# Kernel tuning notes

Hardware: AMD Instinct MI355X
Metric: run time of the kernel (lower is better)

## Reference

```python
import jax, jax.numpy as jnp
import numpy as np

N = 8192
IN_DIM = 256
OUT_DIM = 256  # out_dim//num_heads * num_heads == out_dim
EDGE_PROB = 0.01


def setup_inputs() -> dict:
    key = jax.random.key(0)
    k_adj, k_h, k_q, k_k, k_v = jax.random.split(key, 5)
    # Dense 0/1 adjacency mask, multiplied into the score matrix.
    adj = (jax.random.uniform(k_adj, (N, N)) < EDGE_PROB).astype(jnp.float32)
    h = jax.random.normal(k_h, (N, IN_DIM), dtype=jnp.float32)
    # torch nn.Linear stores weight as [out_features, in_features]; no bias (use_bias=False).
    s = 1.0 / np.sqrt(IN_DIM)
    Wq = jax.random.normal(k_q, (OUT_DIM, IN_DIM), dtype=jnp.float32) * s
    Wk = jax.random.normal(k_k, (OUT_DIM, IN_DIM), dtype=jnp.float32) * s
    Wv = jax.random.normal(k_v, (OUT_DIM, IN_DIM), dtype=jnp.float32) * s
    return {"adj": adj, "h": h, "Wq": Wq, "Wk": Wk, "Wv": Wv}


def reference(adj, h, Wq, Wk, Wv):
    # Q_h, K_h, V_h: [N, out_dim]
    Q_h = h @ Wq.T
    K_h = h @ Wk.T
    V_h = h @ Wv.T
    scale = 1.0 / jnp.sqrt(jnp.asarray(h.shape[1], dtype=h.dtype))
    # Scores masked multiplicatively by adjacency (faithful to source: zeros,
    # not -inf, so non-edges still contribute exp(0) after softmax).
    A_tilde = scale * (Q_h @ K_h.T) * adj            # [N, N]
    attention = jax.nn.softmax(A_tilde, axis=1)       # softmax over dim 1
    X_tilde = attention @ V_h                         # [N, out_dim]
    return X_tilde
```

## Files before the change

kernel.cpp:

```cpp
#include <hip/hip_runtime.h>


#define NN  8192
#define DIM 256
#define SCALE 0.0625f
#define CAP 128

typedef __attribute__((ext_vector_type(8))) short short8;
typedef __attribute__((ext_vector_type(4))) float f32x4;
typedef __attribute__((ext_vector_type(4))) unsigned int u32x4;

__device__ __forceinline__ unsigned short f2bf(float f) {
    union { float f; unsigned u; } v; v.f = f;
    unsigned u = v.u;
    unsigned r = (u + 0x7fffu + ((u >> 16) & 1u)) >> 16;
    return (unsigned short)r;
}
__device__ __forceinline__ float bf2f(unsigned short s) {
    union { unsigned u; float f; } v; v.u = ((unsigned)s) << 16;
    return v.f;
}
__device__ __forceinline__ float dw_lo(unsigned u) {
    union { unsigned u; float f; } v; v.u = u << 16; return v.f;
}
__device__ __forceinline__ float dw_hi(unsigned u) {
    union { unsigned u; float f; } v; v.u = u & 0xffff0000u; return v.f;
}

__global__ __launch_bounds__(256) void prep_kernel(
    const float* __restrict__ h, const float* __restrict__ Wq,
    const float* __restrict__ Wk, const float* __restrict__ Wv,
    unsigned short* __restrict__ h_bf, unsigned short* __restrict__ w_bf)
{
    int b = blockIdx.x, t = threadIdx.x;
    if (b < 2048) {
        int idx = (b * 256 + t) * 4;
        float4 v = *(const float4*)(h + idx);
        ushort4 o; o.x = f2bf(v.x); o.y = f2bf(v.y); o.z = f2bf(v.z); o.w = f2bf(v.w);
        *(ushort4*)(h_bf + idx) = o;
    } else {
        int idx = ((b - 2048) * 256 + t) * 4;
        int w = idx >> 16;
        int offn = idx & 65535;
        const float* src = (w == 0) ? Wq : (w == 1) ? Wk : Wv;
        float4 v = *(const float4*)(src + offn);
        ushort4 o; o.x = f2bf(v.x); o.y = f2bf(v.y); o.z = f2bf(v.z); o.w = f2bf(v.w);
        *(ushort4*)(w_bf + idx) = o;
    }
}

__global__ __launch_bounds__(256) void proj_gemm(
    const unsigned short* __restrict__ h_bf, const unsigned short* __restrict__ w_bf,
    float* __restrict__ Q, unsigned short* __restrict__ Kb, unsigned short* __restrict__ Vb)
{
    __shared__ unsigned short sB[256][40];
    const int mb = blockIdx.x, p = blockIdx.y;
    const unsigned short* W = w_bf + (p << 16);
    const int tid = threadIdx.x, wave = tid >> 6, lane = tid & 63;

    f32x4 acc[16];
#pragma unroll
    for (int f = 0; f < 16; ++f) acc[f] = (f32x4)(0.0f);

    const int arow = mb * 64 + wave * 16 + (lane & 15);
    const int ko   = (lane >> 4) * 8;

    for (int kk = 0; kk < 256; kk += 32) {
        __syncthreads();
        {
            const uint4* src = (const uint4*)(W + tid * 256 + kk);
            uint4* dst = (uint4*)(&sB[tid][0]);
            dst[0] = src[0]; dst[1] = src[1]; dst[2] = src[2]; dst[3] = src[3];
        }
        __syncthreads();
        short8 a = *(const short8*)(h_bf + (size_t)arow * 256 + kk + ko);
#pragma unroll
        for (int f = 0; f < 16; ++f) {
            short8 b = *(const short8*)(&sB[f * 16 + (lane & 15)][ko]);
            acc[f] = __builtin_amdgcn_mfma_f32_16x16x32_bf16(a, b, acc[f], 0, 0, 0);
        }
    }

    const int orow = mb * 64 + wave * 16 + ((lane >> 4) << 2);
    const int ocol = lane & 15;
    if (p == 0) {
#pragma unroll
        for (int f = 0; f < 16; ++f)
#pragma unroll
            for (int r = 0; r < 4; ++r)
                Q[(size_t)(orow + r) * 256 + f * 16 + ocol] = acc[f][r];
    } else {
        unsigned short* dstb = (p == 1) ? Kb : Vb;
#pragma unroll
        for (int f = 0; f < 16; ++f)
#pragma unroll
            for (int r = 0; r < 4; ++r)
                dstb[(size_t)(orow + r) * 256 + f * 16 + ocol] = f2bf(acc[f][r]);
    }
}

__global__ __launch_bounds__(256) void vsum_partial(
    const unsigned short* __restrict__ Vb, float* __restrict__ partial)
{
    int b = blockIdx.x, t = threadIdx.x;
    float s = 0.0f;
    for (int r = 0; r < 64; ++r)
        s += bf2f(Vb[(size_t)(b * 64 + r) * 256 + t]);
    partial[b * 256 + t] = s;
}
__global__ __launch_bounds__(256) void vsum_final(
    const float* __restrict__ partial, float* __restrict__ Vsum)
{
    int t = threadIdx.x;
    float s = 0.0f;
    for (int b = 0; b < 128; ++b) s += partial[b * 256 + t];
    Vsum[t] = s;
}

__global__ __launch_bounds__(256) void attn_main(
    const float* __restrict__ adj, const float* __restrict__ Q,
    const unsigned short* __restrict__ Kb, const unsigned short* __restrict__ Vb,
    const float* __restrict__ Vsum, float* __restrict__ out)
{
    __shared__ int   s_idx[4][CAP];
    __shared__ float s_acc[4][256];
    __shared__ float s_den[4];

    const int i    = blockIdx.x;
    const int tid  = threadIdx.x;
    const int lane = tid & 63;
    const int wave = tid >> 6;

    const f32x4* arow = (const f32x4*)(adj + (size_t)i * NN);
    f32x4 av[8];
#pragma unroll
    for (int it = 0; it < 8; ++it)
        av[it] = __builtin_nontemporal_load(arow + (wave * 512 + it * 64 + lane));

    const unsigned long long lt = (1ull << lane) - 1ull;
    int off = 0;
#pragma unroll
    for (int it = 0; it < 8; ++it) {
        const int colbase = (wave * 512 + it * 64 + lane) * 4;
#pragma unroll
        for (int c = 0; c < 4; ++c) {
            bool nz = (av[it][c] != 0.0f);
            unsigned long long m = __ballot(nz);
            if (nz) s_idx[wave][off + __popcll(m & lt)] = colbase + c;
            off += __popcll(m);
        }
    }

    const float* Qi = Q + (size_t)i * DIM + (lane & 15) * 16;
    f32x4 q0 = *(const f32x4*)(Qi);
    f32x4 q1 = *(const f32x4*)(Qi + 4);
    f32x4 q2 = *(const f32x4*)(Qi + 8);
    f32x4 q3 = *(const f32x4*)(Qi + 12);

    const int g = lane >> 4;
    float acc0 = 0.f, acc1 = 0.f, acc2 = 0.f, acc3 = 0.f, den = 0.f;
    const int rounds = (off + 3) >> 2;

#pragma unroll 2
    for (int r = 0; r < rounds; ++r) {
        const int kb0 = r * 4;
        int jg0 = (kb0 + 0 < off) ? s_idx[wave][kb0 + 0] : 0;
        int jg1 = (kb0 + 1 < off) ? s_idx[wave][kb0 + 1] : 0;
        int jg2 = (kb0 + 2 < off) ? s_idx[wave][kb0 + 2] : 0;
        int jg3 = (kb0 + 3 < off) ? s_idx[wave][kb0 + 3] : 0;

        const bool myv = (kb0 + g) < off;
        const int  myj = (g == 0) ? jg0 : (g == 1) ? jg1 : (g == 2) ? jg2 : jg3;

        const u32x4* kp = (const u32x4*)(Kb + (size_t)myj * DIM + (lane & 15) * 16);
        u32x4 ka = kp[0];
        u32x4 kc = kp[1];

        ushort4 v0 = *(const ushort4*)(Vb + (size_t)jg0 * DIM + lane * 4);
        ushort4 v1 = *(const ushort4*)(Vb + (size_t)jg1 * DIM + lane * 4);
        ushort4 v2 = *(const ushort4*)(Vb + (size_t)jg2 * DIM + lane * 4);
        ushort4 v3 = *(const ushort4*)(Vb + (size_t)jg3 * DIM + lane * 4);

        float d0 = q0[0] * dw_lo(ka[0]);
        float d1 = q0[1] * dw_hi(ka[0]);
        float d2 = q0[2] * dw_lo(ka[1]);
        float d3 = q0[3] * dw_hi(ka[1]);
        d0 = fmaf(q1[0], dw_lo(ka[2]), d0);
        d1 = fmaf(q1[1], dw_hi(ka[2]), d1);
        d2 = fmaf(q1[2], dw_lo(ka[3]), d2);
        d3 = fmaf(q1[3], dw_hi(ka[3]), d3);
        d0 = fmaf(q2[0], dw_lo(kc[0]), d0);
        d1 = fmaf(q2[1], dw_hi(kc[0]), d1);
        d2 = fmaf(q2[2], dw_lo(kc[1]), d2);
        d3 = fmaf(q2[3], dw_hi(kc[1]), d3);
        d0 = fmaf(q3[0], dw_lo(kc[2]), d0);
        d1 = fmaf(q3[1], dw_hi(kc[2]), d1);
        d2 = fmaf(q3[2], dw_lo(kc[3]), d2);
        d3 = fmaf(q3[3], dw_hi(kc[3]), d3);
        float d = (d0 + d1) + (d2 + d3);

        d += __shfl_xor(d, 1);
        d += __shfl_xor(d, 2);
        d += __shfl_xor(d, 4);
        d += __shfl_xor(d, 8);

        float e = myv ? (__expf(SCALE * d) - 1.0f) : 0.0f;

        float e0 = __shfl(e, 0);
        float e1 = __shfl(e, 16);
        float e2 = __shfl(e, 32);
        float e3 = __shfl(e, 48);
        den += (e0 + e1) + (e2 + e3);

        acc0 = fmaf(e0, bf2f(v0.x), acc0); acc1 = fmaf(e0, bf2f(v0.y), acc1);
        acc2 = fmaf(e0, bf2f(v0.z), acc2); acc3 = fmaf(e0, bf2f(v0.w), acc3);
        acc0 = fmaf(e1, bf2f(v1.x), acc0); acc1 = fmaf(e1, bf2f(v1.y), acc1);
        acc2 = fmaf(e1, bf2f(v1.z), acc2); acc3 = fmaf(e1, bf2f(v1.w), acc3);
        acc0 = fmaf(e2, bf2f(v2.x), acc0); acc1 = fmaf(e2, bf2f(v2.y), acc1);
        acc2 = fmaf(e2, bf2f(v2.z), acc2); acc3 = fmaf(e2, bf2f(v2.w), acc3);
        acc0 = fmaf(e3, bf2f(v3.x), acc0); acc1 = fmaf(e3, bf2f(v3.y), acc1);
        acc2 = fmaf(e3, bf2f(v3.z), acc2); acc3 = fmaf(e3, bf2f(v3.w), acc3);
    }

    f32x4 accv = {acc0, acc1, acc2, acc3};
    *(f32x4*)(&s_acc[wave][lane * 4]) = accv;
    if (lane == 0) s_den[wave] = den;
    __syncthreads();

    float a = (s_acc[0][tid] + s_acc[1][tid]) + (s_acc[2][tid] + s_acc[3][tid]);
    float dn = (s_den[0] + s_den[1]) + (s_den[2] + s_den[3]);
    out[(size_t)i * DIM + tid] = (Vsum[tid] + a) / (8192.0f + dn);
}

extern "C" void kernel_launch(void* const* d_in, const int* in_sizes, int n_in,
                              void* d_out, int out_size, void* d_ws, size_t ws_size,
                              hipStream_t stream)
{
    const float* adj = (const float*)d_in[0];
    const float* h   = (const float*)d_in[1];
    const float* Wq  = (const float*)d_in[2];
    const float* Wk  = (const float*)d_in[3];
    const float* Wv  = (const float*)d_in[4];
    float* out = (float*)d_out;

    char* ws = (char*)d_ws;
    size_t off = 0;
    unsigned short* p_hbf = (unsigned short*)(ws + off); off += (size_t)NN * DIM * 2;
    unsigned short* p_wbf = (unsigned short*)(ws + off); off += (size_t)3 * DIM * DIM * 2;
    off = (off + 1023) & ~(size_t)1023;
    float*          p_Q   = (float*)(ws + off);          off += (size_t)NN * DIM * 4;
    unsigned short* p_Kb  = (unsigned short*)(ws + off); off += (size_t)NN * DIM * 2;
    unsigned short* p_Vb  = (unsigned short*)(ws + off); off += (size_t)NN * DIM * 2;
    float*          p_par = (float*)(ws + off);          off += (size_t)128 * DIM * 4;
    float*          p_vs  = (float*)(ws + off);          off += DIM * 4;
    (void)ws_size; (void)in_sizes; (void)n_in; (void)out_size;

    prep_kernel<<<2240, 256, 0, stream>>>(h, Wq, Wk, Wv, p_hbf, p_wbf);
    proj_gemm<<<dim3(128, 3), 256, 0, stream>>>(p_hbf, p_wbf, p_Q, p_Kb, p_Vb);
    vsum_partial<<<128, 256, 0, stream>>>(p_Vb, p_par);
    vsum_final<<<1, 256, 0, stream>>>(p_par, p_vs);
    attn_main<<<NN, 256, 0, stream>>>(adj, p_Q, p_Kb, p_Vb, p_vs, out);
}
```

Baseline: 133.6 us.

## Warp-specialize attention into adjacency-loading producers and sparse-attention consumers

The attention kernel now processes 16 rows per 512-thread block. Four producer waves prefetch adjacency rows into registers and compact the nonzero column indices into double-buffered shared memory. Meanwhile four consumer waves compute the sparse scores and value accumulation for the previous row. The goal is to overlap the streaming read of the adjacency matrix with the gather-and-compute phase. In exchange the grid is much smaller, there are several block barriers per row, and the per-wave index capacity shrinks, which can cut the number of memory requests in flight.

```diff
diff --git a/kernel.cpp b/kernel.cpp
--- a/kernel.cpp
+++ b/kernel.cpp
@@ -4,7 +4,8 @@
 #define NN  8192
 #define DIM 256
 #define SCALE 0.0625f
-#define CAP 128
+#define CAP 96
+#define RPB 16
 
 typedef __attribute__((ext_vector_type(8))) short short8;
 typedef __attribute__((ext_vector_type(4))) float f32x4;
@@ -117,119 +118,166 @@
     Vsum[t] = s;
 }
 
-__global__ __launch_bounds__(256) void attn_main(
+#define LOADROW(av, row)                                                          \
+    {                                                                             \
+        const f32x4* ar_ = (const f32x4*)(adj + (size_t)(row) * NN);              \
+        _Pragma("unroll")                                                         \
+        for (int it_ = 0; it_ < 8; ++it_)                                         \
+            av[it_] = __builtin_nontemporal_load(ar_ + (pw * 512 + it_ * 64 + lane)); \
+    }
+
+#define COMPACT(av, b)                                                            \
+    {                                                                             \
+        int off_ = 0;                                                             \
+        _Pragma("unroll")                                                         \
+        for (int it_ = 0; it_ < 8; ++it_) {                                       \
+            const int colbase_ = (pw * 512 + it_ * 64 + lane) * 4;                \
+            _Pragma("unroll")                                                     \
+            for (int c_ = 0; c_ < 4; ++c_) {                                      \
+                bool nz_ = (av[it_][c_] != 0.0f);                                 \
+                unsigned long long m_ = __ballot(nz_);                            \
+                if (nz_) s_idx[b][pw][off_ + __popcll(m_ & lt)] = colbase_ + c_;  \
+                off_ += __popcll(m_);                                             \
+            }                                                                     \
+        }                                                                         \
+        if (lane == 0) s_cnt[b][pw] = off_;                                       \
+    }
+
+__global__ __launch_bounds__(512, 4) void attn_main(
     const float* __restrict__ adj, const float* __restrict__ Q,
     const unsigned short* __restrict__ Kb, const unsigned short* __restrict__ Vb,
     const float* __restrict__ Vsum, float* __restrict__ out)
 {
-    __shared__ int   s_idx[4][CAP];
-    __shared__ float s_acc[4][256];
+    __shared__ int   s_idx[2][4][CAP];
+    __shared__ int   s_cnt[2][4];
+    __shared__ float s_pacc[4][256];
     __shared__ float s_den[4];
 
-    const int i    = blockIdx.x;
     const int tid  = threadIdx.x;
     const int lane = tid & 63;
     const int wave = tid >> 6;
-
-    const f32x4* arow = (const f32x4*)(adj + (size_t)i * NN);
-    f32x4 av[8];
-#pragma unroll
-    for (int it = 0; it < 8; ++it)
-        av[it] = __builtin_nontemporal_load(arow + (wave * 512 + it * 64 + lane));
-
+    const int i0   = blockIdx.x * RPB;
+    const bool prod = (wave >= 4);
+    const int pw   = wave & 3;
     const unsigned long long lt = (1ull << lane) - 1ull;
-    int off = 0;
-#pragma unroll
-    for (int it = 0; it < 8; ++it) {
-        const int colbase = (wave * 512 + it * 64 + lane) * 4;
-#pragma unroll
-        for (int c = 0; c < 4; ++c) {
-            bool nz = (av[it][c] != 0.0f);
-            unsigned long long m = __ballot(nz);
-            if (nz) s_idx[wave][off + __popcll(m & lt)] = colbase + c;
-            off += __popcll(m);
-        }
-    }
-
-    const float* Qi = Q + (size_t)i * DIM + (lane & 15) * 16;
-    f32x4 q0 = *(const f32x4*)(Qi);
-    f32x4 q1 = *(const f32x4*)(Qi + 4);
-    f32x4 q2 = *(const f32x4*)(Qi + 8);
-    f32x4 q3 = *(const f32x4*)(Qi + 12);
-
-    const int g = lane >> 4;
-    float acc0 = 0.f, acc1 = 0.f, acc2 = 0.f, acc3 = 0.f, den = 0.f;
-    const int rounds = (off + 3) >> 2;
+
+    const float vsum_reg = (tid < 256) ? Vsum[tid] : 0.0f;
+
+    auto consume = [&](int b, int row) {
+        const int cnt = s_cnt[b][pw];
+        const float* Qi = Q + (size_t)row * DIM + (lane & 15) * 16;
+        f32x4 q0 = *(const f32x4*)(Qi);
+        f32x4 q1 = *(const f32x4*)(Qi + 4);
+        f32x4 q2 = *(const f32x4*)(Qi + 8);
+        f32x4 q3 = *(const f32x4*)(Qi + 12);
+
+        const int g = lane >> 4;
+        float acc0 = 0.f, acc1 = 0.f, acc2 = 0.f, acc3 = 0.f, den = 0.f;
+        const int rounds = (cnt + 3) >> 2;
 
 #pragma unroll 2
-    for (int r = 0; r < rounds; ++r) {
-        const int kb0 = r * 4;
-        int jg0 = (kb0 + 0 < off) ? s_idx[wave][kb0 + 0] : 0;
-        int jg1 = (kb0 + 1 < off) ? s_idx[wave][kb0 + 1] : 0;
-        int jg2 = (kb0 + 2 < off) ? s_idx[wave][kb0 + 2] : 0;
-        int jg3 = (kb0 + 3 < off) ? s_idx[wave][kb0 + 3] : 0;
-
-        const bool myv = (kb0 + g) < off;
-        const int  myj = (g == 0) ? jg0 : (g == 1) ? jg1 : (g == 2) ? jg2 : jg3;
-
-        const u32x4* kp = (const u32x4*)(Kb + (size_t)myj * DIM + (lane & 15) * 16);
-        u32x4 ka = kp[0];
-        u32x4 kc = kp[1];
-
-        ushort4 v0 = *(const ushort4*)(Vb + (size_t)jg0 * DIM + lane * 4);
-        ushort4 v1 = *(const ushort4*)(Vb + (size_t)jg1 * DIM + lane * 4);
-        ushort4 v2 = *(const ushort4*)(Vb + (size_t)jg2 * DIM + lane * 4);
-        ushort4 v3 = *(const ushort4*)(Vb + (size_t)jg3 * DIM + lane * 4);
-
-        float d0 = q0[0] * dw_lo(ka[0]);
-        float d1 = q0[1] * dw_hi(ka[0]);
-        float d2 = q0[2] * dw_lo(ka[1]);
-        float d3 = q0[3] * dw_hi(ka[1]);
-        d0 = fmaf(q1[0], dw_lo(ka[2]), d0);
-        d1 = fmaf(q1[1], dw_hi(ka[2]), d1);
-        d2 = fmaf(q1[2], dw_lo(ka[3]), d2);
-        d3 = fmaf(q1[3], dw_hi(ka[3]), d3);
-        d0 = fmaf(q2[0], dw_lo(kc[0]), d0);
-        d1 = fmaf(q2[1], dw_hi(kc[0]), d1);
-        d2 = fmaf(q2[2], dw_lo(kc[1]), d2);
-        d3 = fmaf(q2[3], dw_hi(kc[1]), d3);
-        d0 = fmaf(q3[0], dw_lo(kc[2]), d0);
-        d1 = fmaf(q3[1], dw_hi(kc[2]), d1);
-        d2 = fmaf(q3[2], dw_lo(kc[3]), d2);
-        d3 = fmaf(q3[3], dw_hi(kc[3]), d3);
-        float d = (d0 + d1) + (d2 + d3);
-
-        d += __shfl_xor(d, 1);
-        d += __shfl_xor(d, 2);
-        d += __shfl_xor(d, 4);
-        d += __shfl_xor(d, 8);
-
-        float e = myv ? (__expf(SCALE * d) - 1.0f) : 0.0f;
-
-        float e0 = __shfl(e, 0);
-        float e1 = __shfl(e, 16);
-        float e2 = __shfl(e, 32);
-        float e3 = __shfl(e, 48);
-        den += (e0 + e1) + (e2 + e3);
-
-        acc0 = fmaf(e0, bf2f(v0.x), acc0); acc1 = fmaf(e0, bf2f(v0.y), acc1);
-        acc2 = fmaf(e0, bf2f(v0.z), acc2); acc3 = fmaf(e0, bf2f(v0.w), acc3);
-        acc0 = fmaf(e1, bf2f(v1.x), acc0); acc1 = fmaf(e1, bf2f(v1.y), acc1);
-        acc2 = fmaf(e1, bf2f(v1.z), acc2); acc3 = fmaf(e1, bf2f(v1.w), acc3);
-        acc0 = fmaf(e2, bf2f(v2.x), acc0); acc1 = fmaf(e2, bf2f(v2.y), acc1);
-        acc2 = fmaf(e2, bf2f(v2.z), acc2); acc3 = fmaf(e2, bf2f(v2.w), acc3);
-        acc0 = fmaf(e3, bf2f(v3.x), acc0); acc1 = fmaf(e3, bf2f(v3.y), acc1);
-        acc2 = fmaf(e3, bf2f(v3.z), acc2); acc3 = fmaf(e3, bf2f(v3.w), acc3);
-    }
-
-    f32x4 accv = {acc0, acc1, acc2, acc3};
-    *(f32x4*)(&s_acc[wave][lane * 4]) = accv;
-    if (lane == 0) s_den[wave] = den;
+        for (int r = 0; r < rounds; ++r) {
+            const int kb0 = r * 4;
+            int jg0 = (kb0 + 0 < cnt) ? s_idx[b][pw][kb0 + 0] : 0;
+            int jg1 = (kb0 + 1 < cnt) ? s_idx[b][pw][kb0 + 1] : 0;
+            int jg2 = (kb0 + 2 < cnt) ? s_idx[b][pw][kb0 + 2] : 0;
+            int jg3 = (kb0 + 3 < cnt) ? s_idx[b][pw][kb0 + 3] : 0;
+
+            const bool myv = (kb0 + g) < cnt;
+            const int  myj = (g == 0) ? jg0 : (g == 1) ? jg1 : (g == 2) ? jg2 : jg3;
+
+            const u32x4* kp = (const u32x4*)(Kb + (size_t)myj * DIM + (lane & 15) * 16);
+            u32x4 ka = kp[0];
+            u32x4 kc = kp[1];
+
+            ushort4 v0 = *(const ushort4*)(Vb + (size_t)jg0 * DIM + lane * 4);
+            ushort4 v1 = *(const ushort4*)(Vb + (size_t)jg1 * DIM + lane * 4);
+            ushort4 v2 = *(const ushort4*)(Vb + (size_t)jg2 * DIM + lane * 4);
+            ushort4 v3 = *(const ushort4*)(Vb + (size_t)jg3 * DIM + lane * 4);
+
+            float d0 = q0[0] * dw_lo(ka[0]);
+            float d1 = q0[1] * dw_hi(ka[0]);
+            float d2 = q0[2] * dw_lo(ka[1]);
+            float d3 = q0[3] * dw_hi(ka[1]);
+            d0 = fmaf(q1[0], dw_lo(ka[2]), d0);
+            d1 = fmaf(q1[1], dw_hi(ka[2]), d1);
+            d2 = fmaf(q1[2], dw_lo(ka[3]), d2);
+            d3 = fmaf(q1[3], dw_hi(ka[3]), d3);
+            d0 = fmaf(q2[0], dw_lo(kc[0]), d0);
+            d1 = fmaf(q2[1], dw_hi(kc[0]), d1);
+            d2 = fmaf(q2[2], dw_lo(kc[1]), d2);
+            d3 = fmaf(q2[3], dw_hi(kc[1]), d3);
+            d0 = fmaf(q3[0], dw_lo(kc[2]), d0);
+            d1 = fmaf(q3[1], dw_hi(kc[2]), d1);
+            d2 = fmaf(q3[2], dw_lo(kc[3]), d2);
+            d3 = fmaf(q3[3], dw_hi(kc[3]), d3);
+            float d = (d0 + d1) + (d2 + d3);
+
+            d += __shfl_xor(d, 1);
+            d += __shfl_xor(d, 2);
+            d += __shfl_xor(d, 4);
+            d += __shfl_xor(d, 8);
+
+            float e = myv ? (__expf(SCALE * d) - 1.0f) : 0.0f;
+
+            float e0 = __shfl(e, 0);
+            float e1 = __shfl(e, 16);
+            float e2 = __shfl(e, 32);
+            float e3 = __shfl(e, 48);
+            den += (e0 + e1) + (e2 + e3);
+
+            acc0 = fmaf(e0, bf2f(v0.x), acc0); acc1 = fmaf(e0, bf2f(v0.y), acc1);
+            acc2 = fmaf(e0, bf2f(v0.z), acc2); acc3 = fmaf(e0, bf2f(v0.w), acc3);
+            acc0 = fmaf(e1, bf2f(v1.x), acc0); acc1 = fmaf(e1, bf2f(v1.y), acc1);
+            acc2 = fmaf(e1, bf2f(v1.z), acc2); acc3 = fmaf(e1, bf2f(v1.w), acc3);
+            acc0 = fmaf(e2, bf2f(v2.x), acc0); acc1 = fmaf(e2, bf2f(v2.y), acc1);
+            acc2 = fmaf(e2, bf2f(v2.z), acc2); acc3 = fmaf(e2, bf2f(v2.w), acc3);
+            acc0 = fmaf(e3, bf2f(v3.x), acc0); acc1 = fmaf(e3, bf2f(v3.y), acc1);
+            acc2 = fmaf(e3, bf2f(v3.z), acc2); acc3 = fmaf(e3, bf2f(v3.w), acc3);
+        }
+
+        f32x4 accv = {acc0, acc1, acc2, acc3};
+        *(f32x4*)(&s_pacc[pw][lane * 4]) = accv;
+        if (lane == 0) s_den[pw] = den;
+    };
+
+    auto writeout = [&](int row) {
+        if (tid < 256) {
+            float a  = (s_pacc[0][tid] + s_pacc[1][tid]) + (s_pacc[2][tid] + s_pacc[3][tid]);
+            float dn = (s_den[0] + s_den[1]) + (s_den[2] + s_den[3]);
+            out[(size_t)row * DIM + tid] = (vsum_reg + a) / (8192.0f + dn);
+        }
+    };
+
+    f32x4 avA[8], avB[8];
+    if (prod) {
+        LOADROW(avA, i0);
+        LOADROW(avB, i0 + 1);
+        COMPACT(avA, 0);
+    }
     __syncthreads();
 
-    float a = (s_acc[0][tid] + s_acc[1][tid]) + (s_acc[2][tid] + s_acc[3][tid]);
-    float dn = (s_den[0] + s_den[1]) + (s_den[2] + s_den[3]);
-    out[(size_t)i * DIM + tid] = (Vsum[tid] + a) / (8192.0f + dn);
+    for (int rr = 0; rr < RPB; rr += 2) {
+        if (prod) {
+            if (rr + 2 < RPB) LOADROW(avA, i0 + rr + 2);
+            COMPACT(avB, 1);
+        } else {
+            consume(0, i0 + rr);
+        }
+        __syncthreads();
+        writeout(i0 + rr);
+        __syncthreads();
+
+        if (prod) {
+            if (rr + 3 < RPB) LOADROW(avB, i0 + rr + 3);
+            if (rr + 2 < RPB) COMPACT(avA, 0);
+        } else {
+            consume(1, i0 + rr + 1);
+        }
+        __syncthreads();
+        writeout(i0 + rr + 1);
+        __syncthreads();
+    }
 }
 
 extern "C" void kernel_launch(void* const* d_in, const int* in_sizes, int n_in,
@@ -259,5 +307,5 @@
     proj_gemm<<<dim3(128, 3), 256, 0, stream>>>(p_hbf, p_wbf, p_Q, p_Kb, p_Vb);
     vsum_partial<<<128, 256, 0, stream>>>(p_Vb, p_par);
     vsum_final<<<1, 256, 0, stream>>>(p_par, p_vs);
-    attn_main<<<NN, 256, 0, stream>>>(adj, p_Q, p_Kb, p_Vb, p_vs, out);
-}
+    attn_main<<<NN / RPB, 512, 0, stream>>>(adj, p_Q, p_Kb, p_Vb, p_vs, out);
+}
```

Result: slower. 208.4 us (+55.9%).

## Split adjacency scan into separate kernel writing compact edge lists

Applied to the files above, without the earlier changes.

Moves the adjacency-row scan and compaction out of the attention kernel into a standalone kernel that processes 8 rows per block, double-buffering row loads so they overlap the ballot compaction. Edge indices are stored as 16-bit values in a global workspace with a per-wave count, and the attention kernel now reads only these compact lists. The goal is to stream the 256 MB adjacency at higher bandwidth, free of the gather-heavy attention work, at the cost of an extra launch and a workspace round trip. It shrinks the per-wave capacity to 96, which risks overflow if a 2048-column segment ever holds more than 96 edges.

```diff
diff --git a/kernel.cpp b/kernel.cpp
--- a/kernel.cpp
+++ b/kernel.cpp
@@ -4,7 +4,8 @@
 #define NN  8192
 #define DIM 256
 #define SCALE 0.0625f
-#define CAP 128
+#define CAP 96
+#define RPA 8
 
 typedef __attribute__((ext_vector_type(8))) short short8;
 typedef __attribute__((ext_vector_type(4))) float f32x4;
@@ -117,38 +118,73 @@
     Vsum[t] = s;
 }
 
-__global__ __launch_bounds__(256) void attn_main(
-    const float* __restrict__ adj, const float* __restrict__ Q,
+#define LOADROW(av, row)                                                              \
+    {                                                                                 \
+        const f32x4* ar_ = (const f32x4*)(adj + (size_t)(row) * NN);                  \
+        _Pragma("unroll")                                                             \
+        for (int it_ = 0; it_ < 8; ++it_)                                             \
+            av[it_] = __builtin_nontemporal_load(ar_ + (pw * 512 + it_ * 64 + lane)); \
+    }
+
+#define COMPACT_G(av, row)                                                            \
+    {                                                                                 \
+        unsigned short* dst_ = eidx + ((size_t)(row) * 4 + pw) * CAP;                 \
+        int off_ = 0;                                                                 \
+        _Pragma("unroll")                                                             \
+        for (int it_ = 0; it_ < 8; ++it_) {                                           \
+            const int colbase_ = (pw * 512 + it_ * 64 + lane) * 4;                    \
+            _Pragma("unroll")                                                         \
+            for (int c_ = 0; c_ < 4; ++c_) {                                          \
+                bool nz_ = (av[it_][c_] != 0.0f);                                     \
+                unsigned long long m_ = __ballot(nz_);                                \
+                if (nz_) dst_[off_ + __popcll(m_ & lt)] = (unsigned short)(colbase_ + c_); \
+                off_ += __popcll(m_);                                                 \
+            }                                                                         \
+        }                                                                             \
+        if (lane == 0) ecnt[(row) * 4 + pw] = off_;                                   \
+    }
+
+__global__ __launch_bounds__(256) void adj_scan(
+    const float* __restrict__ adj,
+    unsigned short* __restrict__ eidx, int* __restrict__ ecnt)
+{
+    const int lane = threadIdx.x & 63;
+    const int pw   = threadIdx.x >> 6;
+    const int r0   = blockIdx.x * RPA;
+    const unsigned long long lt = (1ull << lane) - 1ull;
+
+    f32x4 avA[8], avB[8];
+    LOADROW(avA, r0);
+    LOADROW(avB, r0 + 1);
+
+#pragma unroll
+    for (int rr = 0; rr < RPA; rr += 2) {
+        COMPACT_G(avA, r0 + rr);
+        if (rr + 2 < RPA) LOADROW(avA, r0 + rr + 2);
+        COMPACT_G(avB, r0 + rr + 1);
+        if (rr + 3 < RPA) LOADROW(avB, r0 + rr + 3);
+    }
+}
+
+__global__ __launch_bounds__(256) void attn_edges(
+    const unsigned short* __restrict__ eidx, const int* __restrict__ ecnt,
+    const float* __restrict__ Q,
     const unsigned short* __restrict__ Kb, const unsigned short* __restrict__ Vb,
     const float* __restrict__ Vsum, float* __restrict__ out)
 {
-    __shared__ int   s_idx[4][CAP];
-    __shared__ float s_acc[4][256];
+    __shared__ unsigned short s_idx[4][CAP];
+    __shared__ float s_pacc[4][256];
     __shared__ float s_den[4];
 
     const int i    = blockIdx.x;
     const int tid  = threadIdx.x;
     const int lane = tid & 63;
-    const int wave = tid >> 6;
-
-    const f32x4* arow = (const f32x4*)(adj + (size_t)i * NN);
-    f32x4 av[8];
-#pragma unroll
-    for (int it = 0; it < 8; ++it)
-        av[it] = __builtin_nontemporal_load(arow + (wave * 512 + it * 64 + lane));
-
-    const unsigned long long lt = (1ull << lane) - 1ull;
-    int off = 0;
-#pragma unroll
-    for (int it = 0; it < 8; ++it) {
-        const int colbase = (wave * 512 + it * 64 + lane) * 4;
-#pragma unroll
-        for (int c = 0; c < 4; ++c) {
-            bool nz = (av[it][c] != 0.0f);
-            unsigned long long m = __ballot(nz);
-            if (nz) s_idx[wave][off + __popcll(m & lt)] = colbase + c;
-            off += __popcll(m);
-        }
+    const int pw   = tid >> 6;
+
+    const int cnt = ecnt[i * 4 + pw];
+    {
+        const unsigned* src = (const unsigned*)(eidx + ((size_t)i * 4 + pw) * CAP);
+        if (lane < 48) ((unsigned*)&s_idx[pw][0])[lane] = src[lane];
     }
 
     const float* Qi = Q + (size_t)i * DIM + (lane & 15) * 16;
@@ -159,17 +195,17 @@
 
     const int g = lane >> 4;
     float acc0 = 0.f, acc1 = 0.f, acc2 = 0.f, acc3 = 0.f, den = 0.f;
-    const int rounds = (off + 3) >> 2;
+    const int rounds = (cnt + 3) >> 2;
 
 #pragma unroll 2
     for (int r = 0; r < rounds; ++r) {
         const int kb0 = r * 4;
-        int jg0 = (kb0 + 0 < off) ? s_idx[wave][kb0 + 0] : 0;
-        int jg1 = (kb0 + 1 < off) ? s_idx[wave][kb0 + 1] : 0;
-        int jg2 = (kb0 + 2 < off) ? s_idx[wave][kb0 + 2] : 0;
-        int jg3 = (kb0 + 3 < off) ? s_idx[wave][kb0 + 3] : 0;
-
-        const bool myv = (kb0 + g) < off;
+        int jg0 = (kb0 + 0 < cnt) ? (int)s_idx[pw][kb0 + 0] : 0;
+        int jg1 = (kb0 + 1 < cnt) ? (int)s_idx[pw][kb0 + 1] : 0;
+        int jg2 = (kb0 + 2 < cnt) ? (int)s_idx[pw][kb0 + 2] : 0;
+        int jg3 = (kb0 + 3 < cnt) ? (int)s_idx[pw][kb0 + 3] : 0;
+
+        const bool myv = (kb0 + g) < cnt;
         const int  myj = (g == 0) ? jg0 : (g == 1) ? jg1 : (g == 2) ? jg2 : jg3;
 
         const u32x4* kp = (const u32x4*)(Kb + (size_t)myj * DIM + (lane & 15) * 16);
@@ -223,11 +259,11 @@
     }
 
     f32x4 accv = {acc0, acc1, acc2, acc3};
-    *(f32x4*)(&s_acc[wave][lane * 4]) = accv;
-    if (lane == 0) s_den[wave] = den;
+    *(f32x4*)(&s_pacc[pw][lane * 4]) = accv;
+    if (lane == 0) s_den[pw] = den;
     __syncthreads();
 
-    float a = (s_acc[0][tid] + s_acc[1][tid]) + (s_acc[2][tid] + s_acc[3][tid]);
+    float a  = (s_pacc[0][tid] + s_pacc[1][tid]) + (s_pacc[2][tid] + s_pacc[3][tid]);
     float dn = (s_den[0] + s_den[1]) + (s_den[2] + s_den[3]);
     out[(size_t)i * DIM + tid] = (Vsum[tid] + a) / (8192.0f + dn);
 }
@@ -253,11 +289,14 @@
     unsigned short* p_Vb  = (unsigned short*)(ws + off); off += (size_t)NN * DIM * 2;
     float*          p_par = (float*)(ws + off);          off += (size_t)128 * DIM * 4;
     float*          p_vs  = (float*)(ws + off);          off += DIM * 4;
+    unsigned short* p_ei  = (unsigned short*)(ws + off); off += (size_t)NN * 4 * CAP * 2;
+    int*            p_ec  = (int*)(ws + off);            off += (size_t)NN * 4 * 4;
     (void)ws_size; (void)in_sizes; (void)n_in; (void)out_size;
 
+    adj_scan<<<NN / RPA, 256, 0, stream>>>(adj, p_ei, p_ec);
     prep_kernel<<<2240, 256, 0, stream>>>(h, Wq, Wk, Wv, p_hbf, p_wbf);
     proj_gemm<<<dim3(128, 3), 256, 0, stream>>>(p_hbf, p_wbf, p_Q, p_Kb, p_Vb);
     vsum_partial<<<128, 256, 0, stream>>>(p_Vb, p_par);
     vsum_final<<<1, 256, 0, stream>>>(p_par, p_vs);
-    attn_main<<<NN, 256, 0, stream>>>(adj, p_Q, p_Kb, p_Vb, p_vs, out);
-}
+    attn_edges<<<NN, 256, 0, stream>>>(p_ei, p_ec, p_Q, p_Kb, p_Vb, p_vs, out);
+}
```

Result: slower. 141.3 us (+5.7%).

## Split each attention row across four blocks with bf16 partials and finalize pass

Applied to the files above, without the earlier changes.

Each adjacency row is now processed by four blocks, each covering a quarter of the columns, so the grid grows fourfold and each wave scans only 512 columns with a smaller index buffer stored as ushort. Partial numerators are written in bf16 and denominators in fp32, then a new finalize kernel sums the four partials and applies the softmax normalization. The aim is more parallelism and shorter per-block latency on the adjacency scan. In exchange it adds an extra launch, partial-buffer traffic and bf16 rounding of partial sums, and the per-wave index cap of 64 could overflow on dense rows.

```diff
diff --git a/kernel.cpp b/kernel.cpp
--- a/kernel.cpp
+++ b/kernel.cpp
@@ -4,7 +4,7 @@
 #define NN  8192
 #define DIM 256
 #define SCALE 0.0625f
-#define CAP 128
+#define CAP 64
 
 typedef __attribute__((ext_vector_type(8))) short short8;
 typedef __attribute__((ext_vector_type(4))) float f32x4;
@@ -117,59 +117,68 @@
     Vsum[t] = s;
 }
 
-__global__ __launch_bounds__(256) void attn_main(
+__global__ __launch_bounds__(256) void attn_oct(
     const float* __restrict__ adj, const float* __restrict__ Q,
     const unsigned short* __restrict__ Kb, const unsigned short* __restrict__ Vb,
-    const float* __restrict__ Vsum, float* __restrict__ out)
-{
-    __shared__ int   s_idx[4][CAP];
-    __shared__ float s_acc[4][256];
+    unsigned short* __restrict__ pnum, float* __restrict__ pden)
+{
+    __shared__ unsigned short s_idx[4][CAP];
+    __shared__ float s_q[256];
+    __shared__ float s_pacc[4][256];
     __shared__ float s_den[4];
 
-    const int i    = blockIdx.x;
+    const int bq   = blockIdx.x & 3;
+    const int i    = blockIdx.x >> 2;
     const int tid  = threadIdx.x;
     const int lane = tid & 63;
-    const int wave = tid >> 6;
-
-    const f32x4* arow = (const f32x4*)(adj + (size_t)i * NN);
-    f32x4 av[8];
-#pragma unroll
-    for (int it = 0; it < 8; ++it)
-        av[it] = __builtin_nontemporal_load(arow + (wave * 512 + it * 64 + lane));
-
+    const int w    = tid >> 6;
     const unsigned long long lt = (1ull << lane) - 1ull;
+
+    s_q[tid] = __builtin_nontemporal_load(Q + (size_t)i * DIM + tid);
+
+    const f32x4* arow4 = (const f32x4*)(adj + (size_t)i * NN + bq * 2048 + w * 512);
+    f32x4 av0 = __builtin_nontemporal_load(arow4 + lane);
+    f32x4 av1 = __builtin_nontemporal_load(arow4 + 64 + lane);
+
+    const int jbase = bq * 2048 + w * 512;
     int off = 0;
 #pragma unroll
-    for (int it = 0; it < 8; ++it) {
-        const int colbase = (wave * 512 + it * 64 + lane) * 4;
-#pragma unroll
-        for (int c = 0; c < 4; ++c) {
-            bool nz = (av[it][c] != 0.0f);
-            unsigned long long m = __ballot(nz);
-            if (nz) s_idx[wave][off + __popcll(m & lt)] = colbase + c;
-            off += __popcll(m);
-        }
-    }
-
-    const float* Qi = Q + (size_t)i * DIM + (lane & 15) * 16;
-    f32x4 q0 = *(const f32x4*)(Qi);
-    f32x4 q1 = *(const f32x4*)(Qi + 4);
-    f32x4 q2 = *(const f32x4*)(Qi + 8);
-    f32x4 q3 = *(const f32x4*)(Qi + 12);
+    for (int c = 0; c < 4; ++c) {
+        bool nz = (av0[c] != 0.0f);
+        unsigned long long m = __ballot(nz);
+        if (nz) s_idx[w][off + __popcll(m & lt)] = (unsigned short)(jbase + lane * 4 + c);
+        off += __popcll(m);
+    }
+#pragma unroll
+    for (int c = 0; c < 4; ++c) {
+        bool nz = (av1[c] != 0.0f);
+        unsigned long long m = __ballot(nz);
+        if (nz) s_idx[w][off + __popcll(m & lt)] = (unsigned short)(jbase + 256 + lane * 4 + c);
+        off += __popcll(m);
+    }
+    const int cnt = off;
+
+    __syncthreads();
+
+    const int qo = (lane & 15) * 16;
+    f32x4 q0 = *(const f32x4*)(&s_q[qo]);
+    f32x4 q1 = *(const f32x4*)(&s_q[qo + 4]);
+    f32x4 q2 = *(const f32x4*)(&s_q[qo + 8]);
+    f32x4 q3 = *(const f32x4*)(&s_q[qo + 12]);
 
     const int g = lane >> 4;
     float acc0 = 0.f, acc1 = 0.f, acc2 = 0.f, acc3 = 0.f, den = 0.f;
-    const int rounds = (off + 3) >> 2;
+    const int rounds = (cnt + 3) >> 2;
 
 #pragma unroll 2
     for (int r = 0; r < rounds; ++r) {
         const int kb0 = r * 4;
-        int jg0 = (kb0 + 0 < off) ? s_idx[wave][kb0 + 0] : 0;
-        int jg1 = (kb0 + 1 < off) ? s_idx[wave][kb0 + 1] : 0;
-        int jg2 = (kb0 + 2 < off) ? s_idx[wave][kb0 + 2] : 0;
-        int jg3 = (kb0 + 3 < off) ? s_idx[wave][kb0 + 3] : 0;
-
-        const bool myv = (kb0 + g) < off;
+        int jg0 = (kb0 + 0 < cnt) ? (int)s_idx[w][kb0 + 0] : 0;
+        int jg1 = (kb0 + 1 < cnt) ? (int)s_idx[w][kb0 + 1] : 0;
+        int jg2 = (kb0 + 2 < cnt) ? (int)s_idx[w][kb0 + 2] : 0;
+        int jg3 = (kb0 + 3 < cnt) ? (int)s_idx[w][kb0 + 3] : 0;
+
+        const bool myv = (kb0 + g) < cnt;
         const int  myj = (g == 0) ? jg0 : (g == 1) ? jg1 : (g == 2) ? jg2 : jg3;
 
         const u32x4* kp = (const u32x4*)(Kb + (size_t)myj * DIM + (lane & 15) * 16);
@@ -223,13 +232,30 @@
     }
 
     f32x4 accv = {acc0, acc1, acc2, acc3};
-    *(f32x4*)(&s_acc[wave][lane * 4]) = accv;
-    if (lane == 0) s_den[wave] = den;
+    *(f32x4*)(&s_pacc[w][lane * 4]) = accv;
+    if (lane == 0) s_den[w] = den;
     __syncthreads();
 
-    float a = (s_acc[0][tid] + s_acc[1][tid]) + (s_acc[2][tid] + s_acc[3][tid]);
-    float dn = (s_den[0] + s_den[1]) + (s_den[2] + s_den[3]);
-    out[(size_t)i * DIM + tid] = (Vsum[tid] + a) / (8192.0f + dn);
+    float a = (s_pacc[0][tid] + s_pacc[1][tid]) + (s_pacc[2][tid] + s_pacc[3][tid]);
+    __builtin_nontemporal_store(f2bf(a), pnum + (size_t)blockIdx.x * 256 + tid);
+    if (tid == 0) {
+        float dn = (s_den[0] + s_den[1]) + (s_den[2] + s_den[3]);
+        pden[blockIdx.x] = dn;
+    }
+}
+
+__global__ __launch_bounds__(256) void finalize(
+    const unsigned short* __restrict__ pnum, const float* __restrict__ pden,
+    const float* __restrict__ Vsum, float* __restrict__ out)
+{
+    const int i = blockIdx.x, t = threadIdx.x;
+    float num = 0.0f, den = 0.0f;
+#pragma unroll
+    for (int x = 0; x < 4; ++x) {
+        num += bf2f(pnum[(size_t)(i * 4 + x) * 256 + t]);
+        den += pden[i * 4 + x];
+    }
+    out[(size_t)i * DIM + t] = (Vsum[t] + num) / (8192.0f + den);
 }
 
 extern "C" void kernel_launch(void* const* d_in, const int* in_sizes, int n_in,
@@ -253,11 +279,14 @@
     unsigned short* p_Vb  = (unsigned short*)(ws + off); off += (size_t)NN * DIM * 2;
     float*          p_par = (float*)(ws + off);          off += (size_t)128 * DIM * 4;
     float*          p_vs  = (float*)(ws + off);          off += DIM * 4;
+    unsigned short* p_pn  = (unsigned short*)(ws + off); off += (size_t)NN * 4 * 256 * 2;
+    float*          p_pd  = (float*)(ws + off);          off += (size_t)NN * 4 * 4;
     (void)ws_size; (void)in_sizes; (void)n_in; (void)out_size;
 
     prep_kernel<<<2240, 256, 0, stream>>>(h, Wq, Wk, Wv, p_hbf, p_wbf);
     proj_gemm<<<dim3(128, 3), 256, 0, stream>>>(p_hbf, p_wbf, p_Q, p_Kb, p_Vb);
     vsum_partial<<<128, 256, 0, stream>>>(p_Vb, p_par);
     vsum_final<<<1, 256, 0, stream>>>(p_par, p_vs);
-    attn_main<<<NN, 256, 0, stream>>>(adj, p_Q, p_Kb, p_Vb, p_vs, out);
-}
+    attn_oct<<<NN * 4, 256, 0, stream>>>(adj, p_Q, p_Kb, p_Vb, p_pn, p_pd);
+    finalize<<<NN, 256, 0, stream>>>(p_pn, p_pd, p_vs, out);
+}
```

New measurement: 130.8 us. -2.1%, faster.
